# Kernel tuning notes

Hardware: AMD Instinct MI355X
Metric: run time of the kernel (lower is better)

The kernel has to match this reference:

```python
import jax, jax.numpy as jnp
import numpy as np

H = 1024      # hidden_dim
S = 32768     # seq_len


def setup_inputs() -> dict:
    key = jax.random.key(0)
    k1, k2, k3, k4, k5 = jax.random.split(key, 5)
    hidden = jax.random.normal(k1, (1, 2 * H), dtype=jnp.float32)
    encoder_output = jax.random.normal(k2, (S, H), dtype=jnp.float32)
    # nn.Linear default init scale ~ 1/sqrt(fan_in)
    attn_w = jax.random.normal(k3, (H, 3 * H), dtype=jnp.float32) / np.sqrt(3 * H)
    attn_b = jax.random.normal(k4, (H,), dtype=jnp.float32) / np.sqrt(3 * H)
    v_w = jax.random.normal(k5, (1, H), dtype=jnp.float32) / np.sqrt(H)
    return {"hidden": hidden, "encoder_output": encoder_output,
            "attn_w": attn_w, "attn_b": attn_b, "v_w": v_w}


def reference(hidden, encoder_output, attn_w, attn_b, v_w):
    seq_len = encoder_output.shape[0]
    h_rep = jnp.broadcast_to(hidden, (seq_len, hidden.shape[1]))  # repeat(seq_len, 1)
    cat = jnp.concatenate([h_rep, encoder_output], axis=1)        # [S, 3H]
    energy = jnp.tanh(cat @ attn_w.T + attn_b)                    # [S, H]
    attention = (energy @ v_w.T).squeeze()                        # [S]
    return jax.nn.softmax(attention, axis=0)
```

## Files before the change

kernel.cpp:

```cpp
#include <hip/hip_runtime.h>
#include <hip/hip_bf16.h>

#define H  1024
#define S  32768
#define H2 2048
#define H3 3072

typedef __attribute__((ext_vector_type(8))) short bf16x8;
typedef __attribute__((ext_vector_type(4))) float f32x4;

__device__ __forceinline__ unsigned short f2bf(float f) {
    unsigned u = __float_as_uint(f);
    u += 0x7fffu + ((u >> 16) & 1u);
    return (unsigned short)(u >> 16);
}

__device__ __forceinline__ unsigned cvt_pk(float lo, float hi) {
    __hip_bfloat162 h = __float22bfloat162_rn(make_float2(lo, hi));
    unsigned u;
    __builtin_memcpy(&u, &h, 4);
    return u;
}

__device__ __forceinline__ void async_copy16(const void* g, void* l) {
    __builtin_amdgcn_global_load_lds(
        (const __attribute__((address_space(1))) unsigned int*)g,
        (__attribute__((address_space(3))) unsigned int*)l,
        16, 0, 0);
}

__global__ void prep_w2(const float* __restrict__ attn_w, unsigned short* __restrict__ w2b) {
    int idx4 = blockIdx.x * 256 + threadIdx.x;
    int n = idx4 >> 8;
    int c = (idx4 & 255) * 4;
    float4 f = *(const float4*)(attn_w + (size_t)n * H3 + H2 + c);
    ushort4 u;
    u.x = f2bf(f.x); u.y = f2bf(f.y); u.z = f2bf(f.z); u.w = f2bf(f.w);
    *(ushort4*)(w2b + (size_t)n * H + c) = u;
}

__global__ void prep_d(const float* __restrict__ hidden, const float* __restrict__ attn_w,
                       const float* __restrict__ attn_b, float* __restrict__ dvec) {
    int wv = threadIdx.x >> 6, lane = threadIdx.x & 63;
    int row = blockIdx.x * 4 + wv;
    const float* wrow = attn_w + (size_t)row * H3;
    float s = 0.f;
    #pragma unroll
    for (int j = 0; j < 32; ++j) {
        int k = lane + j * 64;
        s += wrow[k] * hidden[k];
    }
    #pragma unroll
    for (int m = 1; m <= 32; m <<= 1) s += __shfl_xor(s, m);
    if (lane == 0) dvec[row] = s + attn_b[row];
}

__global__ __launch_bounds__(256, 2) void attn_gemm(
        const float* __restrict__ enc, const unsigned short* __restrict__ w2b,
        const float* __restrict__ dvec, const float* __restrict__ vw,
        float* __restrict__ logits) {
    __shared__ unsigned short Atile[128 * 32];
    __shared__ unsigned short Btile[128 * 32];

    const int tid = threadIdx.x;
    const int rowBlock = blockIdx.x & 255;
    const int colBlock = blockIdx.x >> 8;

    const int lane = tid & 63;
    const int wv = tid >> 6;
    const int waveM = wv >> 1, waveN = wv & 1;
    const int quad = lane >> 4, l16 = lane & 15;

    f32x4 acc[4][4];
    #pragma unroll
    for (int mi = 0; mi < 4; ++mi)
        #pragma unroll
        for (int ni = 0; ni < 4; ++ni)
            acc[mi][ni] = (f32x4){0.f, 0.f, 0.f, 0.f};

    const int arow = tid >> 3;
    const int akc  = (tid & 7) * 4;
    const size_t encRowBase = (size_t)(rowBlock * 128) * H;

    const unsigned short* Abase = Atile + (waveM * 64 + l16) * 32 + quad * 8;
    const unsigned short* Bbase = Btile + (waveN * 64 + l16) * 32 + quad * 8;

    for (int kt = 0; kt < 32; ++kt) {
        const int k0 = kt * 32;

        #pragma unroll
        for (int p = 0; p < 2; ++p) {
            int c = p * 256 + tid;
            int n = c >> 2, kk = (c & 3) * 8;
            async_copy16(w2b + (size_t)(colBlock * 128 + n) * H + k0 + kk,
                         (char*)Btile + (size_t)c * 16);
        }

        float4 av[4];
        #pragma unroll
        for (int p = 0; p < 4; ++p) {
            int row = arow + p * 32;
            av[p] = *(const float4*)(enc + encRowBase + (size_t)row * H + k0 + akc);
        }
        #pragma unroll
        for (int p = 0; p < 4; ++p) {
            int row = arow + p * 32;
            uint2 u;
            u.x = cvt_pk(av[p].x, av[p].y);
            u.y = cvt_pk(av[p].z, av[p].w);
            *(uint2*)(Atile + row * 32 + akc) = u;
        }

        __syncthreads();

        bf16x8 af[4], bfr[4];
        #pragma unroll
        for (int i = 0; i < 4; ++i) {
            af[i]  = *(const bf16x8*)(Abase + i * 16 * 32);
            bfr[i] = *(const bf16x8*)(Bbase + i * 16 * 32);
        }
        #pragma unroll
        for (int mi = 0; mi < 4; ++mi)
            #pragma unroll
            for (int ni = 0; ni < 4; ++ni)
                acc[mi][ni] = __builtin_amdgcn_mfma_f32_16x16x32_bf16(
                    af[mi], bfr[ni], acc[mi][ni], 0, 0, 0);

        __syncthreads();
    }

    float rowsum[4][4];
    #pragma unroll
    for (int mi = 0; mi < 4; ++mi)
        #pragma unroll
        for (int r = 0; r < 4; ++r) rowsum[mi][r] = 0.f;

    #pragma unroll
    for (int ni = 0; ni < 4; ++ni) {
        int colg = colBlock * 128 + waveN * 64 + ni * 16 + l16;
        float dv = dvec[colg];
        float vv = vw[colg];
        #pragma unroll
        for (int mi = 0; mi < 4; ++mi)
            #pragma unroll
            for (int r = 0; r < 4; ++r)
                rowsum[mi][r] += tanhf(acc[mi][ni][r] + dv) * vv;
    }

    #pragma unroll
    for (int mi = 0; mi < 4; ++mi)
        #pragma unroll
        for (int r = 0; r < 4; ++r) {
            float s = rowsum[mi][r];
            s += __shfl_xor(s, 1);
            s += __shfl_xor(s, 2);
            s += __shfl_xor(s, 4);
            s += __shfl_xor(s, 8);
            rowsum[mi][r] = s;
        }

    if (l16 == 0) {
        int rbase = rowBlock * 128 + waveM * 64 + quad * 4;
        #pragma unroll
        for (int mi = 0; mi < 4; ++mi)
            #pragma unroll
            for (int r = 0; r < 4; ++r)
                atomicAdd(&logits[rbase + mi * 16 + r], rowsum[mi][r]);
    }
}

__global__ __launch_bounds__(1024) void softmax_k(float* __restrict__ x) {
    __shared__ float red[16];
    const int tid = threadIdx.x;
    const int lane = tid & 63, wv = tid >> 6;

    float v[32];
    float m = -1e30f;
    #pragma unroll
    for (int i = 0; i < 32; ++i) {
        v[i] = x[tid + (i << 10)];
        m = fmaxf(m, v[i]);
    }
    #pragma unroll
    for (int o = 1; o < 64; o <<= 1) m = fmaxf(m, __shfl_xor(m, o));
    if (lane == 0) red[wv] = m;
    __syncthreads();
    #pragma unroll
    for (int i = 0; i < 16; ++i) m = fmaxf(m, red[i]);
    __syncthreads();

    float s = 0.f;
    #pragma unroll
    for (int i = 0; i < 32; ++i) {
        v[i] = expf(v[i] - m);
        s += v[i];
    }
    #pragma unroll
    for (int o = 1; o < 64; o <<= 1) s += __shfl_xor(s, o);
    if (lane == 0) red[wv] = s;
    __syncthreads();
    float tot = 0.f;
    #pragma unroll
    for (int i = 0; i < 16; ++i) tot += red[i];
    float inv = 1.0f / tot;

    #pragma unroll
    for (int i = 0; i < 32; ++i) x[tid + (i << 10)] = v[i] * inv;
}

extern "C" void kernel_launch(void* const* d_in, const int* in_sizes, int n_in,
                              void* d_out, int out_size, void* d_ws, size_t ws_size,
                              hipStream_t stream) {
    const float* hidden = (const float*)d_in[0];
    const float* enc    = (const float*)d_in[1];
    const float* attn_w = (const float*)d_in[2];
    const float* attn_b = (const float*)d_in[3];
    const float* v_w    = (const float*)d_in[4];
    float* out = (float*)d_out;

    unsigned short* w2b = (unsigned short*)d_ws;
    float* dvec = (float*)((char*)d_ws + (size_t)H * H * 2);

    hipMemsetAsync(d_out, 0, (size_t)S * sizeof(float), stream);

    prep_w2<<<dim3(1024), dim3(256), 0, stream>>>(attn_w, w2b);
    prep_d<<<dim3(256), dim3(256), 0, stream>>>(hidden, attn_w, attn_b, dvec);
    attn_gemm<<<dim3(2048), dim3(256), 0, stream>>>(enc, w2b, dvec, v_w, out);
    softmax_k<<<dim3(1), dim3(1024), 0, stream>>>(out);
}
```

Baseline: 330.3 us.

## Pre-convert encoder to bf16 and stream both GEMM tiles via async LDS loads

Adds a pre-pass that converts the whole encoder matrix to bf16 in workspace, merged into one prep kernel with the weight conversion and bias-vector computation. When the workspace is large enough, the GEMM then loads both A and B tiles with async global-to-LDS copies instead of a per-tile fp32 load plus convert. This removes the redundant fp32 reloads across the 8 column blocks, at the cost of an extra 128MB read and 64MB write pass. It also replaces tanhf with an exp-based fast tanh.

```diff
diff --git a/kernel.cpp b/kernel.cpp
--- a/kernel.cpp
+++ b/kernel.cpp
@@ -22,6 +22,11 @@
     return u;
 }
 
+__device__ __forceinline__ float tanh_fast(float x) {
+    float e = __expf(2.0f * x);
+    return 1.0f - 2.0f / (e + 1.0f);
+}
+
 __device__ __forceinline__ void async_copy16(const void* g, void* l) {
     __builtin_amdgcn_global_load_lds(
         (const __attribute__((address_space(1))) unsigned int*)g,
@@ -29,20 +34,35 @@
         16, 0, 0);
 }
 
-__global__ void prep_w2(const float* __restrict__ attn_w, unsigned short* __restrict__ w2b) {
-    int idx4 = blockIdx.x * 256 + threadIdx.x;
-    int n = idx4 >> 8;
-    int c = (idx4 & 255) * 4;
-    float4 f = *(const float4*)(attn_w + (size_t)n * H3 + H2 + c);
-    ushort4 u;
-    u.x = f2bf(f.x); u.y = f2bf(f.y); u.z = f2bf(f.z); u.w = f2bf(f.w);
-    *(ushort4*)(w2b + (size_t)n * H + c) = u;
-}
-
-__global__ void prep_d(const float* __restrict__ hidden, const float* __restrict__ attn_w,
-                       const float* __restrict__ attn_b, float* __restrict__ dvec) {
+__global__ void prep_all(const float* __restrict__ enc, const float* __restrict__ attn_w,
+                         const float* __restrict__ attn_b, const float* __restrict__ hidden,
+                         unsigned short* __restrict__ ebf, unsigned short* __restrict__ w2b,
+                         float* __restrict__ dvec, int do_enc) {
+    int b = blockIdx.x;
+    if (do_enc) {
+        if (b < 32768) {
+            size_t idx4 = (size_t)b * 256 + threadIdx.x;
+            float4 f = ((const float4*)enc)[idx4];
+            ushort4 u;
+            u.x = f2bf(f.x); u.y = f2bf(f.y); u.z = f2bf(f.z); u.w = f2bf(f.w);
+            ((ushort4*)ebf)[idx4] = u;
+            return;
+        }
+        b -= 32768;
+    }
+    if (b < 1024) {
+        int idx4 = b * 256 + threadIdx.x;
+        int n = idx4 >> 8;
+        int c = (idx4 & 255) * 4;
+        float4 f = *(const float4*)(attn_w + (size_t)n * H3 + H2 + c);
+        ushort4 u;
+        u.x = f2bf(f.x); u.y = f2bf(f.y); u.z = f2bf(f.z); u.w = f2bf(f.w);
+        *(ushort4*)(w2b + (size_t)n * H + c) = u;
+        return;
+    }
+    b -= 1024;
     int wv = threadIdx.x >> 6, lane = threadIdx.x & 63;
-    int row = blockIdx.x * 4 + wv;
+    int row = b * 4 + wv;
     const float* wrow = attn_w + (size_t)row * H3;
     float s = 0.f;
     #pragma unroll
@@ -55,80 +75,10 @@
     if (lane == 0) dvec[row] = s + attn_b[row];
 }
 
-__global__ __launch_bounds__(256, 2) void attn_gemm(
-        const float* __restrict__ enc, const unsigned short* __restrict__ w2b,
-        const float* __restrict__ dvec, const float* __restrict__ vw,
-        float* __restrict__ logits) {
-    __shared__ unsigned short Atile[128 * 32];
-    __shared__ unsigned short Btile[128 * 32];
-
-    const int tid = threadIdx.x;
-    const int rowBlock = blockIdx.x & 255;
-    const int colBlock = blockIdx.x >> 8;
-
-    const int lane = tid & 63;
-    const int wv = tid >> 6;
-    const int waveM = wv >> 1, waveN = wv & 1;
-    const int quad = lane >> 4, l16 = lane & 15;
-
-    f32x4 acc[4][4];
-    #pragma unroll
-    for (int mi = 0; mi < 4; ++mi)
-        #pragma unroll
-        for (int ni = 0; ni < 4; ++ni)
-            acc[mi][ni] = (f32x4){0.f, 0.f, 0.f, 0.f};
-
-    const int arow = tid >> 3;
-    const int akc  = (tid & 7) * 4;
-    const size_t encRowBase = (size_t)(rowBlock * 128) * H;
-
-    const unsigned short* Abase = Atile + (waveM * 64 + l16) * 32 + quad * 8;
-    const unsigned short* Bbase = Btile + (waveN * 64 + l16) * 32 + quad * 8;
-
-    for (int kt = 0; kt < 32; ++kt) {
-        const int k0 = kt * 32;
-
-        #pragma unroll
-        for (int p = 0; p < 2; ++p) {
-            int c = p * 256 + tid;
-            int n = c >> 2, kk = (c & 3) * 8;
-            async_copy16(w2b + (size_t)(colBlock * 128 + n) * H + k0 + kk,
-                         (char*)Btile + (size_t)c * 16);
-        }
-
-        float4 av[4];
-        #pragma unroll
-        for (int p = 0; p < 4; ++p) {
-            int row = arow + p * 32;
-            av[p] = *(const float4*)(enc + encRowBase + (size_t)row * H + k0 + akc);
-        }
-        #pragma unroll
-        for (int p = 0; p < 4; ++p) {
-            int row = arow + p * 32;
-            uint2 u;
-            u.x = cvt_pk(av[p].x, av[p].y);
-            u.y = cvt_pk(av[p].z, av[p].w);
-            *(uint2*)(Atile + row * 32 + akc) = u;
-        }
-
-        __syncthreads();
-
-        bf16x8 af[4], bfr[4];
-        #pragma unroll
-        for (int i = 0; i < 4; ++i) {
-            af[i]  = *(const bf16x8*)(Abase + i * 16 * 32);
-            bfr[i] = *(const bf16x8*)(Bbase + i * 16 * 32);
-        }
-        #pragma unroll
-        for (int mi = 0; mi < 4; ++mi)
-            #pragma unroll
-            for (int ni = 0; ni < 4; ++ni)
-                acc[mi][ni] = __builtin_amdgcn_mfma_f32_16x16x32_bf16(
-                    af[mi], bfr[ni], acc[mi][ni], 0, 0, 0);
-
-        __syncthreads();
-    }
-
+__device__ __forceinline__ void epilogue(const f32x4 acc[4][4], const float* __restrict__ dvec,
+                                         const float* __restrict__ vw, float* __restrict__ logits,
+                                         int rowBlock, int colBlock, int waveM, int waveN,
+                                         int quad, int l16) {
     float rowsum[4][4];
     #pragma unroll
     for (int mi = 0; mi < 4; ++mi)
@@ -144,7 +94,7 @@
         for (int mi = 0; mi < 4; ++mi)
             #pragma unroll
             for (int r = 0; r < 4; ++r)
-                rowsum[mi][r] += tanhf(acc[mi][ni][r] + dv) * vv;
+                rowsum[mi][r] += tanh_fast(acc[mi][ni][r] + dv) * vv;
     }
 
     #pragma unroll
@@ -167,6 +117,139 @@
             for (int r = 0; r < 4; ++r)
                 atomicAdd(&logits[rbase + mi * 16 + r], rowsum[mi][r]);
     }
+}
+
+__global__ __launch_bounds__(256, 2) void attn_gemm_fast(
+        const unsigned short* __restrict__ ebf, const unsigned short* __restrict__ w2b,
+        const float* __restrict__ dvec, const float* __restrict__ vw,
+        float* __restrict__ logits) {
+    __shared__ unsigned short Atile[128 * 32];
+    __shared__ unsigned short Btile[128 * 32];
+
+    const int tid = threadIdx.x;
+    const int rowBlock = blockIdx.x & 255;
+    const int colBlock = blockIdx.x >> 8;
+
+    const int lane = tid & 63;
+    const int wv = tid >> 6;
+    const int waveM = wv >> 1, waveN = wv & 1;
+    const int quad = lane >> 4, l16 = lane & 15;
+
+    f32x4 acc[4][4];
+    #pragma unroll
+    for (int mi = 0; mi < 4; ++mi)
+        #pragma unroll
+        for (int ni = 0; ni < 4; ++ni)
+            acc[mi][ni] = (f32x4){0.f, 0.f, 0.f, 0.f};
+
+    const unsigned short* Abase = Atile + (waveM * 64 + l16) * 32 + quad * 8;
+    const unsigned short* Bbase = Btile + (waveN * 64 + l16) * 32 + quad * 8;
+
+    const size_t aRow0 = (size_t)(rowBlock * 128) * H;
+    const size_t bRow0 = (size_t)(colBlock * 128) * H;
+
+    for (int kt = 0; kt < 32; ++kt) {
+        const int k0 = kt * 32;
+
+        #pragma unroll
+        for (int p = 0; p < 2; ++p) {
+            int c = p * 256 + tid;
+            int n = c >> 2, kk = (c & 3) * 8;
+            async_copy16(ebf + aRow0 + (size_t)n * H + k0 + kk, (char*)Atile + (size_t)c * 16);
+            async_copy16(w2b + bRow0 + (size_t)n * H + k0 + kk, (char*)Btile + (size_t)c * 16);
+        }
+
+        __syncthreads();
+
+        bf16x8 af[4], bfr[4];
+        #pragma unroll
+        for (int i = 0; i < 4; ++i) {
+            af[i]  = *(const bf16x8*)(Abase + i * 16 * 32);
+            bfr[i] = *(const bf16x8*)(Bbase + i * 16 * 32);
+        }
+        #pragma unroll
+        for (int mi = 0; mi < 4; ++mi)
+            #pragma unroll
+            for (int ni = 0; ni < 4; ++ni)
+                acc[mi][ni] = __builtin_amdgcn_mfma_f32_16x16x32_bf16(
+                    af[mi], bfr[ni], acc[mi][ni], 0, 0, 0);
+
+        __syncthreads();
+    }
+
+    epilogue(acc, dvec, vw, logits, rowBlock, colBlock, waveM, waveN, quad, l16);
+}
+
+__global__ __launch_bounds__(256, 2) void attn_gemm_fb(
+        const float* __restrict__ enc, const unsigned short* __restrict__ w2b,
+        const float* __restrict__ dvec, const float* __restrict__ vw,
+        float* __restrict__ logits) {
+    __shared__ unsigned short Atile[128 * 32];
+    __shared__ unsigned short Btile[128 * 32];
+
+    const int tid = threadIdx.x;
+    const int rowBlock = blockIdx.x & 255;
+    const int colBlock = blockIdx.x >> 8;
+
+    const int lane = tid & 63;
+    const int wv = tid >> 6;
+    const int waveM = wv >> 1, waveN = wv & 1;
+    const int quad = lane >> 4, l16 = lane & 15;
+
+    f32x4 acc[4][4];
+    #pragma unroll
+    for (int mi = 0; mi < 4; ++mi)
+        #pragma unroll
+        for (int ni = 0; ni < 4; ++ni)
+            acc[mi][ni] = (f32x4){0.f, 0.f, 0.f, 0.f};
+
+    const int arow = tid >> 3;
+    const int akc  = (tid & 7) * 4;
+    const size_t encRowBase = (size_t)(rowBlock * 128) * H;
+
+    const unsigned short* Abase = Atile + (waveM * 64 + l16) * 32 + quad * 8;
+    const unsigned short* Bbase = Btile + (waveN * 64 + l16) * 32 + quad * 8;
+
+    for (int kt = 0; kt < 32; ++kt) {
+        const int k0 = kt * 32;
+        #pragma unroll
+        for (int p = 0; p < 2; ++p) {
+            int c = p * 256 + tid;
+            int n = c >> 2, kk = (c & 3) * 8;
+            async_copy16(w2b + (size_t)(colBlock * 128 + n) * H + k0 + kk,
+                         (char*)Btile + (size_t)c * 16);
+        }
+        float4 av[4];
+        #pragma unroll
+        for (int p = 0; p < 4; ++p)
+            av[p] = *(const float4*)(enc + encRowBase + (size_t)(arow + p * 32) * H + k0 + akc);
+        #pragma unroll
+        for (int p = 0; p < 4; ++p) {
+            uint2 u;
+            u.x = cvt_pk(av[p].x, av[p].y);
+            u.y = cvt_pk(av[p].z, av[p].w);
+            *(uint2*)(Atile + (arow + p * 32) * 32 + akc) = u;
+        }
+
+        __syncthreads();
+
+        bf16x8 af[4], bfr[4];
+        #pragma unroll
+        for (int i = 0; i < 4; ++i) {
+            af[i]  = *(const bf16x8*)(Abase + i * 16 * 32);
+            bfr[i] = *(const bf16x8*)(Bbase + i * 16 * 32);
+        }
+        #pragma unroll
+        for (int mi = 0; mi < 4; ++mi)
+            #pragma unroll
+            for (int ni = 0; ni < 4; ++ni)
+                acc[mi][ni] = __builtin_amdgcn_mfma_f32_16x16x32_bf16(
+                    af[mi], bfr[ni], acc[mi][ni], 0, 0, 0);
+
+        __syncthreads();
+    }
+
+    epilogue(acc, dvec, vw, logits, rowBlock, colBlock, waveM, waveN, quad, l16);
 }
 
 __global__ __launch_bounds__(1024) void softmax_k(float* __restrict__ x) {
@@ -218,13 +301,25 @@
     const float* v_w    = (const float*)d_in[4];
     float* out = (float*)d_out;
 
-    unsigned short* w2b = (unsigned short*)d_ws;
-    float* dvec = (float*)((char*)d_ws + (size_t)H * H * 2);
+    const size_t EBF_BYTES = (size_t)S * H * 2;
+    const size_t W2_BYTES  = (size_t)H * H * 2;
+    const bool fast = ws_size >= EBF_BYTES + W2_BYTES + 4096;
 
     hipMemsetAsync(d_out, 0, (size_t)S * sizeof(float), stream);
 
-    prep_w2<<<dim3(1024), dim3(256), 0, stream>>>(attn_w, w2b);
-    prep_d<<<dim3(256), dim3(256), 0, stream>>>(hidden, attn_w, attn_b, dvec);
-    attn_gemm<<<dim3(2048), dim3(256), 0, stream>>>(enc, w2b, dvec, v_w, out);
+    if (fast) {
+        unsigned short* ebf = (unsigned short*)d_ws;
+        unsigned short* w2b = (unsigned short*)((char*)d_ws + EBF_BYTES);
+        float* dvec = (float*)((char*)d_ws + EBF_BYTES + W2_BYTES);
+        prep_all<<<dim3(32768 + 1024 + 256), dim3(256), 0, stream>>>(
+            enc, attn_w, attn_b, hidden, ebf, w2b, dvec, 1);
+        attn_gemm_fast<<<dim3(2048), dim3(256), 0, stream>>>(ebf, w2b, dvec, v_w, out);
+    } else {
+        unsigned short* w2b = (unsigned short*)d_ws;
+        float* dvec = (float*)((char*)d_ws + W2_BYTES);
+        prep_all<<<dim3(1024 + 256), dim3(256), 0, stream>>>(
+            enc, attn_w, attn_b, hidden, nullptr, w2b, dvec, 0);
+        attn_gemm_fb<<<dim3(2048), dim3(256), 0, stream>>>(enc, w2b, dvec, v_w, out);
+    }
     softmax_k<<<dim3(1), dim3(1024), 0, stream>>>(out);
 }
```

New measurement: 312.8 us. -5.3%, faster.
